# Optimization experiments

Hardware: AMD Instinct MI355X
Metric: run time of the kernel (lower is better)

## Reference

```python
import jax, jax.numpy as jnp
import numpy as np

EMBED_DIM = 512
B, N = 8, 2048


def setup_inputs() -> dict:
    key = jax.random.key(0)
    ks = jax.random.split(key, 9)
    d = EMBED_DIM
    s = 1.0 / np.sqrt(d)
    return {
        "x": jax.random.normal(ks[0], (B, N, d), dtype=jnp.float32),
        "Wq": jax.random.uniform(ks[1], (d, d), jnp.float32, -s, s),
        "bq": jax.random.uniform(ks[2], (d,), jnp.float32, -s, s),
        "Wk": jax.random.uniform(ks[3], (d, d), jnp.float32, -s, s),
        "bk": jax.random.uniform(ks[4], (d,), jnp.float32, -s, s),
        "Wv": jax.random.uniform(ks[5], (d, d), jnp.float32, -s, s),
        "bv": jax.random.uniform(ks[6], (d,), jnp.float32, -s, s),
        "Wo": jax.random.uniform(ks[7], (d, d), jnp.float32, -s, s),
        "bo": jax.random.uniform(ks[8], (d,), jnp.float32, -s, s),
    }


def reference(x, Wq, bq, Wk, bk, Wv, bv, Wo, bo):
    d = x.shape[-1]
    scale = d ** (-0.5)
    q = x @ Wq + bq              # [B, N, D]
    k = x @ Wk + bk
    v = x @ Wv + bv
    attn = jnp.einsum('bnd,bmd->bnm', q, k) * scale  # [B, N, N]
    attn = jax.nn.softmax(attn, axis=-1)
    out = jnp.einsum('bnm,bmd->bnd', attn, v)
    return out @ Wo + bo
```

## Files before the change

kernel.cpp:

```cpp
#include <hip/hip_runtime.h>
#include <hip/hip_bf16.h>
#include <hip/hip_fp8.h>
#include <stdint.h>

typedef __bf16 bf16;
typedef __attribute__((ext_vector_type(8))) short short8;
typedef __attribute__((ext_vector_type(4))) float f32x4;
typedef __attribute__((ext_vector_type(4))) bf16 bf16x4;
typedef __attribute__((ext_vector_type(8))) int int8v;
typedef __attribute__((ext_vector_type(4))) int int4v;

#define DIM 512
#define NBATCH 8
#define SEQ 2048

__device__ __forceinline__ void gld_lds16(const void* g, void* l) {
    __builtin_amdgcn_global_load_lds(
        (const __attribute__((address_space(1))) void*)g,
        (__attribute__((address_space(3))) void*)l,
        16, 0, 0);
}

__device__ __forceinline__ unsigned char f32_to_e4m3(float v) {
#if __has_builtin(__builtin_amdgcn_cvt_pk_fp8_f32)
    return (unsigned char)(__builtin_amdgcn_cvt_pk_fp8_f32(v, v, 0, false) & 0xff);
#else
    return __hip_cvt_float_to_fp8(v, __HIP_SATFINITE, __HIP_E4M3);
#endif
}

template <int MODE, int SWIZ>
__global__ __launch_bounds__(256, 3) void gemm_bt(
    const bf16* __restrict__ A, const bf16* __restrict__ Bt,
    void* __restrict__ Cv, const float* __restrict__ bias,
    int N, int K, long long sC, float alpha, int gx)
{
    __shared__ bf16 smem[32768];
    bf16* Asb = smem;
    bf16* Bsb = smem + 16384;

    int bx, by;
    {
        const unsigned g = blockIdx.x;
        const unsigned xcd = g & 7;
        const unsigned t = g >> 3;
        const unsigned per = (gridDim.x >> 3) / (unsigned)gx;
        by = xcd * per + t / (unsigned)gx;
        bx = t % (unsigned)gx;
    }

    const int tid  = threadIdx.x;
    const int lane = tid & 63;
    const int w    = tid >> 6;
    const int wr   = w >> 1;
    const int wc   = w & 1;
    const int lm   = lane & 15;
    const int lk   = lane >> 4;
    const int fs   = lm & 7;
    const int rq   = tid >> 3;
    const int pc   = tid & 7;
    const int scol = ((pc ^ (rq & 7)) * 8);

    const bf16* Ag = A + (size_t)(by * 128) * K;
    const bf16* Bg = Bt + (size_t)(bx * 128) * K;

    f32x4 acc[4][4];
#pragma unroll
    for (int i = 0; i < 4; ++i)
#pragma unroll
        for (int j = 0; j < 4; ++j)
            acc[i][j] = (f32x4){0.f, 0.f, 0.f, 0.f};

    auto stage = [&](int kb, int buf) {
#pragma unroll
        for (int t = 0; t < 4; ++t) {
            const int r = t * 32 + rq;
            gld_lds16(Ag + (size_t)r * K + kb + scol,
                      Asb + buf * 8192 + t * 2048 + tid * 8);
            gld_lds16(Bg + (size_t)r * K + kb + scol,
                      Bsb + buf * 8192 + t * 2048 + tid * 8);
        }
    };
    auto compute = [&](int buf) {
        const bf16* Ab = Asb + buf * 8192;
        const bf16* Bb = Bsb + buf * 8192;
#pragma unroll
        for (int s = 0; s < 2; ++s) {
            const int u = ((s * 4 + lk) ^ fs) * 8;
            short8 fa[4], fb[4];
#pragma unroll
            for (int i = 0; i < 4; ++i)
                fa[i] = *(const short8*)&Ab[(wr * 64 + i * 16 + lm) * 64 + u];
#pragma unroll
            for (int j = 0; j < 4; ++j)
                fb[j] = *(const short8*)&Bb[(wc * 64 + j * 16 + lm) * 64 + u];
#pragma unroll
            for (int i = 0; i < 4; ++i)
#pragma unroll
                for (int j = 0; j < 4; ++j)
                    acc[i][j] = __builtin_amdgcn_mfma_f32_16x16x32_bf16(
                        fa[i], fb[j], acc[i][j], 0, 0, 0);
        }
    };

    stage(0, 0);
    __syncthreads();
    const int E = K >> 6;
#pragma unroll 2
    for (int e = 0; e < E; ++e) {
        if (e + 1 < E) stage((e + 1) << 6, (e + 1) & 1);
        compute(e & 1);
        __syncthreads();
    }

    if (MODE == 2) {
        float* ft = (float*)smem;
        float* outp = (float*)Cv;
#pragma unroll
        for (int h = 0; h < 2; ++h) {
            if (wr == h) {
#pragma unroll
                for (int i = 0; i < 4; ++i)
#pragma unroll
                    for (int j = 0; j < 4; ++j) {
                        const int col = wc * 64 + j * 16 + lm;
                        const float bv = bias[bx * 128 + col];
#pragma unroll
                        for (int r = 0; r < 4; ++r)
                            ft[(i * 16 + lk * 4 + r) * 132 + col] =
                                acc[i][j][r] + bv;
                    }
            }
            __syncthreads();
            const int rr = tid >> 5, cc = (tid & 31) * 4;
#pragma unroll
            for (int p = 0; p < 8; ++p) {
                const int row = p * 8 + rr;
                *(float4*)&outp[(size_t)(by * 128 + h * 64 + row) * N +
                                bx * 128 + cc] = *(const float4*)&ft[row * 132 + cc];
            }
            __syncthreads();
        }
        return;
    }

#pragma unroll
    for (int i = 0; i < 4; ++i)
#pragma unroll
        for (int j = 0; j < 4; ++j) {
            const int col = bx * 128 + wc * 64 + j * 16 + lm;
            const float bv = bias[col];
#pragma unroll
            for (int r = 0; r < 4; ++r)
                acc[i][j][r] += bv;
        }

    const int sub  = (bx * 128) >> 9;
    const int col0 = (bx * 128) & 511;
    uint8_t* d8 = (uint8_t*)Cv + (size_t)sub * 8388608;
    uint8_t* t8 = (uint8_t*)smem;
#pragma unroll
    for (int h = 0; h < 2; ++h) {
        if (wr == h) {
#pragma unroll
            for (int i = 0; i < 4; ++i)
#pragma unroll
                for (int j = 0; j < 4; ++j)
#pragma unroll
                    for (int r = 0; r < 4; ++r)
                        t8[(i * 16 + lk * 4 + r) * 144 + wc * 64 + j * 16 + lm] =
                            f32_to_e4m3(32.0f * acc[i][j][r]);
        }
        __syncthreads();
        const int rr = tid >> 3, cc = (tid & 7) * 16;
#pragma unroll
        for (int p = 0; p < 2; ++p) {
            const int row = p * 32 + rr;
            const uint4 raw = *(const uint4*)&t8[row * 144 + cc];
            *(uint4*)&d8[(size_t)(by * 128 + h * 64 + row) * 512 + col0 + cc] =
                raw;
        }
        __syncthreads();
    }
}

template <int MODE>
__global__ __launch_bounds__(256, 3) void gemm_mx(
    const uint8_t* __restrict__ A, const uint8_t* __restrict__ Bt,
    void* __restrict__ Cv, float* __restrict__ rsum,
    int N, int K, long long sA, long long sB, long long sC, float alpha,
    int gx)
{
    __shared__ uint8_t smem[32768];
    uint8_t* As = smem;
    uint8_t* Bs = smem + 16384;

    int bx, by, bz;
    {
        const unsigned g = blockIdx.x;
        bz = g & 7;
        const unsigned r = g >> 3;
        bx = r % (unsigned)gx;
        by = r / (unsigned)gx;
    }

    const int tid  = threadIdx.x;
    const int lane = tid & 63;
    const int w    = tid >> 6;
    const int wr   = w >> 1;
    const int wc   = w & 1;
    const int lm   = lane & 15;
    const int lk   = lane >> 4;
    const int rq   = tid >> 3;
    const int pc   = tid & 7;
    const int ssrc = (pc ^ (rq & 7)) * 16;
    const int ca   = ((2 * lk) ^ (lm & 7)) * 16;
    const int cb   = ((2 * lk + 1) ^ (lm & 7)) * 16;

    const size_t z = bz;
    const uint8_t* Ag = A + z * (size_t)sA + (size_t)(by * 128) * K;
    const uint8_t* Bg = Bt + z * (size_t)sB + (size_t)(bx * 128) * K;

    f32x4 acc[4][4];
#pragma unroll
    for (int i = 0; i < 4; ++i)
#pragma unroll
        for (int j = 0; j < 4; ++j)
            acc[i][j] = (f32x4){0.f, 0.f, 0.f, 0.f};

    for (int kb = 0; kb < K; kb += 128) {
#pragma unroll
        for (int t = 0; t < 4; ++t) {
            const int r = t * 32 + rq;
            gld_lds16(Ag + (size_t)r * K + kb + ssrc, As + t * 4096 + tid * 16);
            gld_lds16(Bg + (size_t)r * K + kb + ssrc, Bs + t * 4096 + tid * 16);
        }
        __syncthreads();

        int8v fa[4];
#pragma unroll
        for (int i = 0; i < 4; ++i) {
            const uint8_t* rp = As + (wr * 64 + i * 16 + lm) * 128;
            const int4v lo = *(const int4v*)(rp + ca);
            const int4v hi = *(const int4v*)(rp + cb);
            fa[i] = (int8v){lo[0], lo[1], lo[2], lo[3], hi[0], hi[1], hi[2], hi[3]};
        }
#pragma unroll
        for (int j = 0; j < 4; ++j) {
            const uint8_t* rp = Bs + (wc * 64 + j * 16 + lm) * 128;
            const int4v lo = *(const int4v*)(rp + ca);
            const int4v hi = *(const int4v*)(rp + cb);
            const int8v fb = (int8v){lo[0], lo[1], lo[2], lo[3],
                                     hi[0], hi[1], hi[2], hi[3]};
#pragma unroll
            for (int i = 0; i < 4; ++i)
                acc[i][j] = __builtin_amdgcn_mfma_scale_f32_16x16x128_f8f6f4(
                    fa[i], fb, acc[i][j], 0, 0, 0, 127, 0, 127);
        }
        __syncthreads();
    }

    const int orow0 = by * 128 + wr * 64;

    if (MODE == 4) {
#pragma unroll
        for (int i = 0; i < 4; ++i) {
            float psum[4] = {0.f, 0.f, 0.f, 0.f};
#pragma unroll
            for (int j = 0; j < 4; ++j)
#pragma unroll
                for (int r = 0; r < 4; ++r) {
                    const float e = __expf(acc[i][j][r] * alpha);
                    acc[i][j][r] = e;
                    psum[r] += e;
                }
#pragma unroll
            for (int m = 1; m < 16; m <<= 1)
#pragma unroll
                for (int r = 0; r < 4; ++r) psum[r] += __shfl_xor(psum[r], m);
            if (lm == 0) {
#pragma unroll
                for (int r = 0; r < 4; ++r)
                    atomicAdd(&rsum[z * SEQ + orow0 + i * 16 + lk * 4 + r],
                              psum[r]);
            }
        }
        uint8_t* dst = (uint8_t*)Cv + z * (size_t)sC;
#pragma unroll
        for (int h = 0; h < 2; ++h) {
            if (wr == h) {
#pragma unroll
                for (int i = 0; i < 4; ++i)
#pragma unroll
                    for (int j = 0; j < 4; ++j)
#pragma unroll
                        for (int r = 0; r < 4; ++r)
                            smem[(i * 16 + lk * 4 + r) * 144 +
                                 wc * 64 + j * 16 + lm] =
                                f32_to_e4m3(acc[i][j][r]);
            }
            __syncthreads();
            const int rr = tid >> 3, cc = (tid & 7) * 16;
#pragma unroll
            for (int p = 0; p < 2; ++p) {
                const int row = p * 32 + rr;
                const uint4 raw = *(const uint4*)&smem[row * 144 + cc];
                *(uint4*)&dst[(size_t)(by * 128 + h * 64 + row) * N +
                              bx * 128 + cc] = raw;
            }
            __syncthreads();
        }
        return;
    }

#pragma unroll
    for (int i = 0; i < 4; ++i) {
        float inv[4];
#pragma unroll
        for (int r = 0; r < 4; ++r)
            inv[r] = 1.0f / (32.0f * rsum[z * SEQ + orow0 + i * 16 + lk * 4 + r]);
#pragma unroll
        for (int j = 0; j < 4; ++j)
#pragma unroll
            for (int r = 0; r < 4; ++r)
                acc[i][j][r] *= inv[r];
    }
    bf16* dst = (bf16*)Cv + z * (size_t)sC;
    bf16* tile = (bf16*)smem;
#pragma unroll
    for (int h = 0; h < 2; ++h) {
        if (wr == h) {
#pragma unroll
            for (int i = 0; i < 4; ++i)
#pragma unroll
                for (int j = 0; j < 4; ++j)
#pragma unroll
                    for (int r = 0; r < 4; ++r)
                        tile[(i * 16 + lk * 4 + r) * 136 + wc * 64 + j * 16 + lm] =
                            (bf16)acc[i][j][r];
        }
        __syncthreads();
        const int rr0 = tid >> 4, cc = (tid & 15) * 8;
#pragma unroll
        for (int p = 0; p < 4; ++p) {
            const int row = p * 16 + rr0;
            const uint4 raw = *(const uint4*)&tile[row * 136 + cc];
            *(uint4*)&dst[(size_t)(by * 128 + h * 64 + row) * N + bx * 128 + cc] =
                raw;
        }
        __syncthreads();
    }
}

__global__ __launch_bounds__(256) void transpose_v8(
    const uint8_t* __restrict__ V, uint8_t* __restrict__ Vt)
{
    __shared__ uint8_t tile[64][68];
    const int b = blockIdx.z, tx = blockIdx.x, ty = blockIdx.y;
    const int t0 = threadIdx.x;
    const int r = t0 >> 2, c0 = (t0 & 3) * 16;
    *(uint4*)&tile[r][c0] =
        *(const uint4*)&V[((size_t)b * SEQ + ty * 64 + r) * 512 + tx * 64 + c0];
    __syncthreads();
    const int o = t0 >> 2, i0 = (t0 & 3) * 16;
    uint4 pk;
    uint8_t* pb = (uint8_t*)&pk;
#pragma unroll
    for (int j = 0; j < 16; ++j) pb[j] = tile[i0 + j][o];
    *(uint4*)&Vt[((size_t)b * 512 + tx * 64 + o) * SEQ + ty * 64 + i0] = pk;
}

__global__ __launch_bounds__(256) void cvt_f32_bf16(
    const float* __restrict__ x, bf16* __restrict__ o, int n4)
{
    const int i = blockIdx.x * 256 + threadIdx.x;
    if (i >= n4) return;
    const float4 v = ((const float4*)x)[i];
    bf16x4 b;
    b[0] = (bf16)v.x; b[1] = (bf16)v.y; b[2] = (bf16)v.z; b[3] = (bf16)v.w;
    ((bf16x4*)o)[i] = b;
}

__global__ __launch_bounds__(256) void transpose4(
    const float* __restrict__ Wq, const float* __restrict__ Wk,
    const float* __restrict__ Wv, const float* __restrict__ Wo,
    bf16* __restrict__ Wcat, bf16* __restrict__ Wto,
    const float* __restrict__ bq, const float* __restrict__ bk,
    const float* __restrict__ bv, float* __restrict__ bcat,
    float* __restrict__ rowsum)
{
    const int widx = blockIdx.z;
    const int t0 = threadIdx.x;
    if (widx == 4) {
        const int idx = (blockIdx.y * 8 + blockIdx.x) * 256 + t0;
        rowsum[idx] = 0.0f;
        if (idx < 1536)
            bcat[idx] = (idx < 512) ? bq[idx]
                      : (idx < 1024) ? bk[idx - 512] : bv[idx - 1024];
        return;
    }
    __shared__ bf16 tile[64][65];
    const float* W = (widx == 0) ? Wq : (widx == 1) ? Wk : (widx == 2) ? Wv : Wo;
    bf16* dst = (widx < 3) ? (Wcat + (size_t)widx * 512 * 512) : Wto;
    const int tx = blockIdx.x, ty = blockIdx.y;
#pragma unroll
    for (int it = 0; it < 16; ++it) {
        const int e = it * 256 + t0;
        const int r = e >> 6, c = e & 63;
        tile[r][c] = (bf16)W[(size_t)(ty * 64 + r) * 512 + tx * 64 + c];
    }
    __syncthreads();
#pragma unroll
    for (int it = 0; it < 16; ++it) {
        const int e = it * 256 + t0;
        const int o = e >> 6, i = e & 63;
        dst[(size_t)(tx * 64 + o) * 512 + ty * 64 + i] = tile[i][o];
    }
}

extern "C" void kernel_launch(void* const* d_in, const int* in_sizes, int n_in,
                              void* d_out, int out_size, void* d_ws, size_t ws_size,
                              hipStream_t stream)
{
    const float* x  = (const float*)d_in[0];
    const float* Wq = (const float*)d_in[1];
    const float* bq = (const float*)d_in[2];
    const float* Wk = (const float*)d_in[3];
    const float* bk = (const float*)d_in[4];
    const float* Wv = (const float*)d_in[5];
    const float* bv = (const float*)d_in[6];
    const float* Wo = (const float*)d_in[7];
    const float* bo = (const float*)d_in[8];
    float* out = (float*)d_out;

    char* ws = (char*)d_ws;
    bf16*    Xb     = (bf16*)(ws);
    bf16*    Ctx    = (bf16*)(ws);
    bf16*    Wcat   = (bf16*)(ws + 16777216);
    bf16*    Wto    = (bf16*)(ws + 18350080);
    float*   bcat   = (float*)(ws + 18874368);
    float*   rowsum = (float*)(ws + 18880512);
    uint8_t* Q8     = (uint8_t*)(ws + 20971520);
    uint8_t* K8     = (uint8_t*)(ws + 29360128);
    uint8_t* V8     = (uint8_t*)(ws + 37748736);
    uint8_t* Vt8    = (uint8_t*)(ws + 54525952);
    uint8_t* S8     = (uint8_t*)(ws + 62914560);

    transpose4<<<dim3(8, 8, 5), 256, 0, stream>>>(
        Wq, Wk, Wv, Wo, Wcat, Wto, bq, bk, bv, bcat, rowsum);
    cvt_f32_bf16<<<8192, 256, 0, stream>>>(x, Xb, 2097152);

    const float scale = 0.044194173824159216f;

    gemm_bt<3, 2><<<1536, 256, 0, stream>>>(
        Xb, Wcat, Q8, bcat, 1536, 512, 0, 1.0f, 12);

    transpose_v8<<<dim3(8, 32, 8), 256, 0, stream>>>(V8, Vt8);

    gemm_mx<4><<<2048, 256, 0, stream>>>(
        Q8, K8, S8, rowsum, 2048, 512,
        2048LL * 512, 2048LL * 512, 2048LL * 2048, scale / 1024.0f, 16);

    gemm_mx<5><<<512, 256, 0, stream>>>(
        S8, Vt8, Ctx, rowsum, 512, 2048,
        2048LL * 2048, 512LL * 2048, 2048LL * 512, 1.0f, 4);

    gemm_bt<2, 2><<<512, 256, 0, stream>>>(
        Ctx, Wto, out, bo, 512, 512, 0, 1.0f, 4);
}
```

Before: 223.4 us.

## Fold output projection into V weights and drop final projection GEMM

Precomputes Wv·Wo and the bias bv·Wo+bo in prep kernels, so the QKV projection directly produces U = x·(Wv·Wo)+b' instead of V. The PV GEMM then writes fp32 output directly, which removes the Ctx round trip and the final output-projection GEMM launch. Costs are a small extra 512×512 GEMM and a serial bias dot-product kernel. Occupancy hints are also dropped from the launch bounds, and because U is quantized to fp8 after folding in Wo, precision may shift.

```diff
diff --git a/kernel.cpp b/kernel.cpp
--- a/kernel.cpp
+++ b/kernel.cpp
@@ -30,23 +30,25 @@
 }
 
 template <int MODE, int SWIZ>
-__global__ __launch_bounds__(256, 3) void gemm_bt(
+__global__ __launch_bounds__(256) void gemm_bt(
     const bf16* __restrict__ A, const bf16* __restrict__ Bt,
     void* __restrict__ Cv, const float* __restrict__ bias,
-    int N, int K, long long sC, float alpha, int gx)
+    int N, int K, int gx)
 {
     __shared__ bf16 smem[32768];
     bf16* Asb = smem;
     bf16* Bsb = smem + 16384;
 
     int bx, by;
-    {
+    if (SWIZ == 2) {
         const unsigned g = blockIdx.x;
         const unsigned xcd = g & 7;
         const unsigned t = g >> 3;
         const unsigned per = (gridDim.x >> 3) / (unsigned)gx;
         by = xcd * per + t / (unsigned)gx;
         bx = t % (unsigned)gx;
+    } else {
+        bx = blockIdx.x; by = blockIdx.y;
     }
 
     const int tid  = threadIdx.x;
@@ -113,47 +115,45 @@
         __syncthreads();
     }
 
-    if (MODE == 2) {
-        float* ft = (float*)smem;
-        float* outp = (float*)Cv;
+#pragma unroll
+    for (int i = 0; i < 4; ++i)
+#pragma unroll
+        for (int j = 0; j < 4; ++j) {
+            const int col = bx * 128 + wc * 64 + j * 16 + lm;
+            const float bv = bias ? bias[col] : 0.0f;
+#pragma unroll
+            for (int r = 0; r < 4; ++r)
+                acc[i][j][r] += bv;
+        }
+
+    if (MODE == 0) {
+        bf16* dst = (bf16*)Cv;
+        const int col0 = bx * 128;
 #pragma unroll
         for (int h = 0; h < 2; ++h) {
             if (wr == h) {
 #pragma unroll
                 for (int i = 0; i < 4; ++i)
 #pragma unroll
-                    for (int j = 0; j < 4; ++j) {
-                        const int col = wc * 64 + j * 16 + lm;
-                        const float bv = bias[bx * 128 + col];
+                    for (int j = 0; j < 4; ++j)
 #pragma unroll
                         for (int r = 0; r < 4; ++r)
-                            ft[(i * 16 + lk * 4 + r) * 132 + col] =
-                                acc[i][j][r] + bv;
-                    }
+                            smem[(i * 16 + lk * 4 + r) * 136 + wc * 64 + j * 16 + lm] =
+                                (bf16)acc[i][j][r];
             }
             __syncthreads();
-            const int rr = tid >> 5, cc = (tid & 31) * 4;
-#pragma unroll
-            for (int p = 0; p < 8; ++p) {
-                const int row = p * 8 + rr;
-                *(float4*)&outp[(size_t)(by * 128 + h * 64 + row) * N +
-                                bx * 128 + cc] = *(const float4*)&ft[row * 132 + cc];
+            const int rr0 = tid >> 4, cc = (tid & 15) * 8;
+#pragma unroll
+            for (int p = 0; p < 4; ++p) {
+                const int row = p * 16 + rr0;
+                const uint4 raw = *(const uint4*)&smem[row * 136 + cc];
+                *(uint4*)&dst[(size_t)(by * 128 + h * 64 + row) * N + col0 + cc] =
+                    raw;
             }
             __syncthreads();
         }
         return;
     }
-
-#pragma unroll
-    for (int i = 0; i < 4; ++i)
-#pragma unroll
-        for (int j = 0; j < 4; ++j) {
-            const int col = bx * 128 + wc * 64 + j * 16 + lm;
-            const float bv = bias[col];
-#pragma unroll
-            for (int r = 0; r < 4; ++r)
-                acc[i][j][r] += bv;
-        }
 
     const int sub  = (bx * 128) >> 9;
     const int col0 = (bx * 128) & 511;
@@ -185,13 +185,13 @@
 }
 
 template <int MODE>
-__global__ __launch_bounds__(256, 3) void gemm_mx(
+__global__ __launch_bounds__(256) void gemm_mx(
     const uint8_t* __restrict__ A, const uint8_t* __restrict__ Bt,
     void* __restrict__ Cv, float* __restrict__ rsum,
     int N, int K, long long sA, long long sB, long long sC, float alpha,
     int gx)
 {
-    __shared__ uint8_t smem[32768];
+    __shared__ uint8_t smem[33792];
     uint8_t* As = smem;
     uint8_t* Bs = smem + 16384;
 
@@ -325,8 +325,8 @@
             for (int r = 0; r < 4; ++r)
                 acc[i][j][r] *= inv[r];
     }
-    bf16* dst = (bf16*)Cv + z * (size_t)sC;
-    bf16* tile = (bf16*)smem;
+    float* dst = (float*)Cv + z * (size_t)sC;
+    float* ft = (float*)smem;
 #pragma unroll
     for (int h = 0; h < 2; ++h) {
         if (wr == h) {
@@ -336,17 +336,16 @@
                 for (int j = 0; j < 4; ++j)
 #pragma unroll
                     for (int r = 0; r < 4; ++r)
-                        tile[(i * 16 + lk * 4 + r) * 136 + wc * 64 + j * 16 + lm] =
-                            (bf16)acc[i][j][r];
-        }
-        __syncthreads();
-        const int rr0 = tid >> 4, cc = (tid & 15) * 8;
-#pragma unroll
-        for (int p = 0; p < 4; ++p) {
-            const int row = p * 16 + rr0;
-            const uint4 raw = *(const uint4*)&tile[row * 136 + cc];
-            *(uint4*)&dst[(size_t)(by * 128 + h * 64 + row) * N + bx * 128 + cc] =
-                raw;
+                        ft[(i * 16 + lk * 4 + r) * 132 + wc * 64 + j * 16 + lm] =
+                            acc[i][j][r];
+        }
+        __syncthreads();
+        const int rr = tid >> 5, cc = (tid & 31) * 4;
+#pragma unroll
+        for (int p = 0; p < 8; ++p) {
+            const int row = p * 8 + rr;
+            *(float4*)&dst[(size_t)(by * 128 + h * 64 + row) * N + bx * 128 + cc] =
+                *(const float4*)&ft[row * 132 + cc];
         }
         __syncthreads();
     }
@@ -381,28 +380,47 @@
     ((bf16x4*)o)[i] = b;
 }
 
-__global__ __launch_bounds__(256) void transpose4(
+__global__ __launch_bounds__(256) void prep(
     const float* __restrict__ Wq, const float* __restrict__ Wk,
     const float* __restrict__ Wv, const float* __restrict__ Wo,
-    bf16* __restrict__ Wcat, bf16* __restrict__ Wto,
+    bf16* __restrict__ Wcat, bf16* __restrict__ Wto, bf16* __restrict__ Wvb,
     const float* __restrict__ bq, const float* __restrict__ bk,
-    const float* __restrict__ bv, float* __restrict__ bcat,
-    float* __restrict__ rowsum)
+    const float* __restrict__ bv, const float* __restrict__ bo,
+    float* __restrict__ bcat, float* __restrict__ rowsum)
 {
     const int widx = blockIdx.z;
     const int t0 = threadIdx.x;
     if (widx == 4) {
         const int idx = (blockIdx.y * 8 + blockIdx.x) * 256 + t0;
         rowsum[idx] = 0.0f;
-        if (idx < 1536)
-            bcat[idx] = (idx < 512) ? bq[idx]
-                      : (idx < 1024) ? bk[idx - 512] : bv[idx - 1024];
+        if (idx < 1024) bcat[idx] = (idx < 512) ? bq[idx] : bk[idx - 512];
         return;
     }
+    if (widx == 5) {
+        const int idx = (blockIdx.y * 8 + blockIdx.x) * 256 + t0;
+        if (idx < 512) {
+            float s = bo[idx];
+#pragma unroll 8
+            for (int k = 0; k < 512; ++k)
+                s += bv[k] * Wo[k * 512 + idx];
+            bcat[1024 + idx] = s;
+        }
+        return;
+    }
+    const int tx = blockIdx.x, ty = blockIdx.y;
+    if (widx == 2) {
+#pragma unroll
+        for (int it = 0; it < 16; ++it) {
+            const int e = it * 256 + t0;
+            const int r = e >> 6, c = e & 63;
+            const size_t lin = (size_t)(ty * 64 + r) * 512 + tx * 64 + c;
+            Wvb[lin] = (bf16)Wv[lin];
+        }
+        return;
+    }
     __shared__ bf16 tile[64][65];
-    const float* W = (widx == 0) ? Wq : (widx == 1) ? Wk : (widx == 2) ? Wv : Wo;
-    bf16* dst = (widx < 3) ? (Wcat + (size_t)widx * 512 * 512) : Wto;
-    const int tx = blockIdx.x, ty = blockIdx.y;
+    const float* W = (widx == 0) ? Wq : (widx == 1) ? Wk : Wo;
+    bf16* dst = (widx == 0) ? Wcat : (widx == 1) ? (Wcat + 512 * 512) : Wto;
 #pragma unroll
     for (int it = 0; it < 16; ++it) {
         const int e = it * 256 + t0;
@@ -435,36 +453,37 @@
 
     char* ws = (char*)d_ws;
     bf16*    Xb     = (bf16*)(ws);
-    bf16*    Ctx    = (bf16*)(ws);
     bf16*    Wcat   = (bf16*)(ws + 16777216);
     bf16*    Wto    = (bf16*)(ws + 18350080);
     float*   bcat   = (float*)(ws + 18874368);
     float*   rowsum = (float*)(ws + 18880512);
+    bf16*    Wvb    = (bf16*)(ws + 18946048);
     uint8_t* Q8     = (uint8_t*)(ws + 20971520);
     uint8_t* K8     = (uint8_t*)(ws + 29360128);
-    uint8_t* V8     = (uint8_t*)(ws + 37748736);
-    uint8_t* Vt8    = (uint8_t*)(ws + 54525952);
+    uint8_t* U8     = (uint8_t*)(ws + 37748736);
+    uint8_t* Ut8    = (uint8_t*)(ws + 54525952);
     uint8_t* S8     = (uint8_t*)(ws + 62914560);
 
-    transpose4<<<dim3(8, 8, 5), 256, 0, stream>>>(
-        Wq, Wk, Wv, Wo, Wcat, Wto, bq, bk, bv, bcat, rowsum);
+    prep<<<dim3(8, 8, 6), 256, 0, stream>>>(
+        Wq, Wk, Wv, Wo, Wcat, Wto, Wvb, bq, bk, bv, bo, bcat, rowsum);
+
+    gemm_bt<0, 0><<<dim3(4, 4), 256, 0, stream>>>(
+        Wto, Wvb, Wcat + 1024 * 512, nullptr, 512, 512, 0);
+
     cvt_f32_bf16<<<8192, 256, 0, stream>>>(x, Xb, 2097152);
 
     const float scale = 0.044194173824159216f;
 
     gemm_bt<3, 2><<<1536, 256, 0, stream>>>(
-        Xb, Wcat, Q8, bcat, 1536, 512, 0, 1.0f, 12);
-
-    transpose_v8<<<dim3(8, 32, 8), 256, 0, stream>>>(V8, Vt8);
+        Xb, Wcat, Q8, bcat, 1536, 512, 12);
+
+    transpose_v8<<<dim3(8, 32, 8), 256, 0, stream>>>(U8, Ut8);
 
     gemm_mx<4><<<2048, 256, 0, stream>>>(
         Q8, K8, S8, rowsum, 2048, 512,
         2048LL * 512, 2048LL * 512, 2048LL * 2048, scale / 1024.0f, 16);
 
     gemm_mx<5><<<512, 256, 0, stream>>>(
-        S8, Vt8, Ctx, rowsum, 512, 2048,
+        S8, Ut8, out, rowsum, 512, 2048,
         2048LL * 2048, 512LL * 2048, 2048LL * 512, 1.0f, 4);
-
-    gemm_bt<2, 2><<<512, 256, 0, stream>>>(
-        Ctx, Wto, out, bo, 512, 512, 0, 1.0f, 4);
-}
+}
```

New measurement: 245.5 us. +9.9%, slower.
